# Performance work log

Measured on AMD Instinct MI355X. Metric: run time of the kernel, lower is better.

Reference implementation:

```python
import jax, jax.numpy as jnp
import numpy as np

B, N, K = 16, 4096, 32

def setup_inputs() -> dict:
    key = jax.random.key(0)
    k0, k1, k2, k3, k4, k5 = jax.random.split(key, 6)
    frames_rot = jax.random.normal(k0, (B, N, 3, 3), jnp.float32)
    frames_trans = jax.random.normal(k1, (B, N, 3), jnp.float32)
    pair_rot = jax.random.normal(k2, (B, N, K, 3, 3), jnp.float32)
    pair_trans = jax.random.normal(k3, (B, N, K, 3), jnp.float32)
    confidences = jax.random.uniform(k4, (B, N, K, 1), jnp.float32)
    topology = jax.random.randint(k5, (B, N, K), 0, N, jnp.int32)
    return {"frames_rot": frames_rot, "frames_trans": frames_trans,
            "pair_rot": pair_rot, "pair_trans": pair_trans,
            "confidences": confidences, "topology": topology}


def _proj_with_svd(m):
    """Kabsch projection of batched [..., 3, 3] matrices onto SO(3) (det=+1)."""
    u, s, vh = jnp.linalg.svd(m, full_matrices=False)
    V = jnp.swapaxes(vh, -1, -2)
    d = jnp.sign(jnp.linalg.det(jnp.matmul(V, jnp.swapaxes(u, -1, -2))))  # [...]
    d3 = jnp.concatenate([jnp.ones(d.shape + (2,), m.dtype), d[..., None]], axis=-1)  # diag(1,1,d)
    # rot = V @ diag(1,1,d) @ u^T
    return jnp.einsum('...ik,...k,...jk->...ij', V, d3, u)


def reference(frames_rot, frames_trans, pair_rot, pair_trans, confidences, topology):
    # gather neighbor frames T_j: [B,N,K,3,3] / [B,N,K,3]
    gather = jax.vmap(lambda f, t: f[t])
    Tj_rot = gather(frames_rot, topology)
    Tj_trans = gather(frames_trans, topology)

    # normalized confidences p_ij over neighbors K
    w = jnp.squeeze(confidences, axis=-1)             # [B,N,K]
    p = w / jnp.sum(w, axis=2, keepdims=True)         # [B,N,K]

    # compose rigids: T_j * T_ji
    comp_rot = jnp.einsum('bnkij,bnkjl->bnkil', Tj_rot, pair_rot)                 # [B,N,K,3,3]
    comp_trans = jnp.einsum('bnkij,bnkj->bnki', Tj_rot, pair_trans) + Tj_trans    # [B,N,K,3]

    # confidence-weighted average over neighbors
    avg_rot = jnp.einsum('bnk,bnkij->bnij', p, comp_rot)    # [B,N,3,3]
    avg_trans = jnp.einsum('bnk,bnki->bni', p, comp_trans)  # [B,N,3]

    # project averaged rot onto SO(3), then invert (transpose) as in the module
    rot = _proj_with_svd(avg_rot)
    rot_inv = jnp.swapaxes(rot, -1, -2)                     # invert_rots of a rotation

    # pack (rot 9 + trans 3) -> [B,N,12]
    return jnp.concatenate([rot_inv.reshape(B, N, 9), avg_trans], axis=-1)
```

## Files before the change

### kernel.cpp

```cpp
#include <hip/hip_runtime.h>
#include <math.h>

#define N_RES 4096
#define KNB 32
#define BN_TOTAL 65536

typedef float v4f __attribute__((ext_vector_type(4)));
typedef int v4i __attribute__((ext_vector_type(4)));

template <int p, int q>
__device__ __forceinline__ void jacobi_rot(float S[3][3], float V[3][3]) {
    float apq = S[p][q];
    if (fabsf(apq) > 1e-20f) {
        float app = S[p][p], aqq = S[q][q];
        float tau = (aqq - app) / (2.0f * apq);
        float tt = (tau >= 0.0f ? 1.0f : -1.0f) / (fabsf(tau) + sqrtf(1.0f + tau * tau));
        float c = 1.0f / sqrtf(1.0f + tt * tt);
        float s = tt * c;
#pragma unroll
        for (int i = 0; i < 3; i++) {
            float Sip = S[i][p], Siq = S[i][q];
            S[i][p] = c * Sip - s * Siq;
            S[i][q] = s * Sip + c * Siq;
        }
#pragma unroll
        for (int i = 0; i < 3; i++) {
            float Spi = S[p][i], Sqi = S[q][i];
            S[p][i] = c * Spi - s * Sqi;
            S[q][i] = s * Spi + c * Sqi;
        }
#pragma unroll
        for (int i = 0; i < 3; i++) {
            float Vip = V[i][p], Viq = V[i][q];
            V[i][p] = c * Vip - s * Viq;
            V[i][q] = s * Vip + c * Viq;
        }
    }
}

template <int A, int Bc>
__device__ __forceinline__ void sort_pair(float lam[3], float V[3][3]) {
    if (lam[A] < lam[Bc]) {
        float tl = lam[A]; lam[A] = lam[Bc]; lam[Bc] = tl;
#pragma unroll
        for (int i = 0; i < 3; i++) {
            float tv = V[i][A]; V[i][A] = V[i][Bc]; V[i][Bc] = tv;
        }
    }
}

__device__ __forceinline__ void project_and_store(const float M[3][3],
                                                  float t0, float t1, float t2,
                                                  float* outp) {
    float S[3][3];
#pragma unroll
    for (int i = 0; i < 3; i++)
#pragma unroll
        for (int j = 0; j < 3; j++)
            S[i][j] = M[0][i] * M[0][j] + M[1][i] * M[1][j] + M[2][i] * M[2][j];
    float V[3][3] = {{1, 0, 0}, {0, 1, 0}, {0, 0, 1}};

#pragma unroll
    for (int sweep = 0; sweep < 4; sweep++) {
        jacobi_rot<0, 1>(S, V);
        jacobi_rot<0, 2>(S, V);
        jacobi_rot<1, 2>(S, V);
    }

    float lam[3] = {S[0][0], S[1][1], S[2][2]};
    sort_pair<0, 1>(lam, V);
    sort_pair<1, 2>(lam, V);
    sort_pair<0, 1>(lam, V);

    float detV = V[0][0] * (V[1][1] * V[2][2] - V[1][2] * V[2][1]) -
                 V[0][1] * (V[1][0] * V[2][2] - V[1][2] * V[2][0]) +
                 V[0][2] * (V[1][0] * V[2][1] - V[1][1] * V[2][0]);
    if (detV < 0.0f) { V[0][2] = -V[0][2]; V[1][2] = -V[1][2]; V[2][2] = -V[2][2]; }

    float Bm[3][3];
#pragma unroll
    for (int i = 0; i < 3; i++)
#pragma unroll
        for (int j = 0; j < 3; j++)
            Bm[i][j] = M[i][0] * V[0][j] + M[i][1] * V[1][j] + M[i][2] * V[2][j];

    float u0[3] = {Bm[0][0], Bm[1][0], Bm[2][0]};
    float n0 = u0[0] * u0[0] + u0[1] * u0[1] + u0[2] * u0[2];
    float rn0 = 1.0f / sqrtf(fmaxf(n0, 1e-24f));
    u0[0] *= rn0; u0[1] *= rn0; u0[2] *= rn0;

    float b1[3] = {Bm[0][1], Bm[1][1], Bm[2][1]};
    float d01 = u0[0] * b1[0] + u0[1] * b1[1] + u0[2] * b1[2];
    float u1[3] = {b1[0] - d01 * u0[0], b1[1] - d01 * u0[1], b1[2] - d01 * u0[2]};
    float n1 = u1[0] * u1[0] + u1[1] * u1[1] + u1[2] * u1[2];
    float rn1 = 1.0f / sqrtf(fmaxf(n1, 1e-24f));
    u1[0] *= rn1; u1[1] *= rn1; u1[2] *= rn1;

    float u2[3] = {u0[1] * u1[2] - u0[2] * u1[1],
                   u0[2] * u1[0] - u0[0] * u1[2],
                   u0[0] * u1[1] - u0[1] * u1[0]};

    float R[9];
#pragma unroll
    for (int i = 0; i < 3; i++) {
        float Ui0 = (i == 0 ? u0[0] : (i == 1 ? u0[1] : u0[2]));
        float Ui1 = (i == 0 ? u1[0] : (i == 1 ? u1[1] : u1[2]));
        float Ui2 = (i == 0 ? u2[0] : (i == 1 ? u2[1] : u2[2]));
#pragma unroll
        for (int j = 0; j < 3; j++)
            R[i * 3 + j] = Ui0 * V[j][0] + Ui1 * V[j][1] + Ui2 * V[j][2];
    }

    v4f* o4 = (v4f*)outp;
    o4[0] = (v4f){R[0], R[1], R[2], R[3]};
    o4[1] = (v4f){R[4], R[5], R[6], R[7]};
    o4[2] = (v4f){R[8], t0, t1, t2};
}

__global__ __launch_bounds__(256) void repack_kernel(
    const float* __restrict__ frames_rot,
    const float* __restrict__ frames_trans,
    float* __restrict__ pk)
{
    int row = blockIdx.x * 256 + threadIdx.x;
    const float* fr = frames_rot + (size_t)row * 9;
    const float* ft = frames_trans + (size_t)row * 3;
    v4f* o = (v4f*)(pk + (size_t)row * 16);
    o[0] = (v4f){fr[0], fr[1], fr[2], fr[3]};
    o[1] = (v4f){fr[4], fr[5], fr[6], fr[7]};
    o[2] = (v4f){fr[8], ft[0], ft[1], ft[2]};
}

__global__ __launch_bounds__(256) void accum_kernel(
    const float* __restrict__ pk,
    const float* __restrict__ pair_rot,
    const float* __restrict__ pair_trans,
    const float* __restrict__ conf,
    const int* __restrict__ topo,
    float* __restrict__ acc)
{
    __shared__ float lds[4 * 768];

    int tid = threadIdx.x;
    int wid = tid >> 6;
    int L = tid & 63;
    int bid = blockIdx.x;

    int xcd = bid & 7;
    int slot = bid >> 3;
    int batch = xcd + ((slot >> 9) << 3);
    int within = slot & 511;
    int elem0 = batch * N_RES + within * 8 + wid * 2;

    int h = L >> 5;
    int k = L & 31;
    int elem_g = elem0 + h;

    float* wlds = lds + wid * 768;

    size_t nidx = (size_t)elem0 * KNB + L;
    float w = __builtin_nontemporal_load(conf + nidx);
    int j = __builtin_nontemporal_load(topo + nidx);

    const v4f* rg = (const v4f*)(pair_rot + (size_t)elem0 * (KNB * 9));
    for (int s = L; s < 144; s += 64) {
        v4f v = __builtin_nontemporal_load(rg + s);
        *(v4f*)(wlds + 4 * s) = v;
    }
    const v4f* tg = (const v4f*)(pair_trans + (size_t)elem0 * (KNB * 3));
    if (L < 48) {
        v4f v = __builtin_nontemporal_load(tg + L);
        *(v4f*)(wlds + 576 + 4 * L) = v;
    }

    const v4f* row = (const v4f*)(pk + ((size_t)batch * N_RES + (size_t)j) * 16);
    v4f fa = row[0], fb = row[1], fc = row[2];
    float r[9] = {fa.x, fa.y, fa.z, fa.w, fb.x, fb.y, fb.z, fb.w, fc.x};
    float tj0 = fc.y, tj1 = fc.z, tj2 = fc.w;

    const float* pr = wlds + h * 288 + k * 9;
    float p[9];
#pragma unroll
    for (int c = 0; c < 9; c++) p[c] = pr[c];
    const float* pt = wlds + 576 + h * 96 + k * 3;
    float q0 = pt[0], q1 = pt[1], q2 = pt[2];

    float Macc[9], tacc[3];
#pragma unroll
    for (int i = 0; i < 3; i++) {
#pragma unroll
        for (int l = 0; l < 3; l++) {
            Macc[i * 3 + l] = w * (r[i * 3 + 0] * p[0 * 3 + l] +
                                   r[i * 3 + 1] * p[1 * 3 + l] +
                                   r[i * 3 + 2] * p[2 * 3 + l]);
        }
        float tji = (i == 0 ? tj0 : (i == 1 ? tj1 : tj2));
        tacc[i] = w * (r[i * 3 + 0] * q0 + r[i * 3 + 1] * q1 +
                       r[i * 3 + 2] * q2 + tji);
    }
    float wsum = w;

#pragma unroll
    for (int st = 1; st <= 16; st <<= 1) {
#pragma unroll
        for (int i = 0; i < 9; i++) Macc[i] += __shfl_xor(Macc[i], st);
#pragma unroll
        for (int i = 0; i < 3; i++) tacc[i] += __shfl_xor(tacc[i], st);
        wsum += __shfl_xor(wsum, st);
    }

    if (k == 0) {
        v4f* o = (v4f*)(acc + (size_t)elem_g * 16);
        o[0] = (v4f){Macc[0], Macc[1], Macc[2], Macc[3]};
        o[1] = (v4f){Macc[4], Macc[5], Macc[6], Macc[7]};
        o[2] = (v4f){Macc[8], tacc[0], tacc[1], tacc[2]};
        o[3] = (v4f){wsum, 0.0f, 0.0f, 0.0f};
    }
}

__global__ __launch_bounds__(256) void solve_kernel(
    const float* __restrict__ acc,
    float* __restrict__ out)
{
    int elem = blockIdx.x * 256 + threadIdx.x;
    const v4f* a4 = (const v4f*)(acc + (size_t)elem * 16);
    v4f A0 = a4[0], A1 = a4[1], A2 = a4[2], A3 = a4[3];
    float inv_w = 1.0f / fmaxf(A3.x, 1e-20f);
    float M[3][3] = {{A0.x * inv_w, A0.y * inv_w, A0.z * inv_w},
                     {A0.w * inv_w, A1.x * inv_w, A1.y * inv_w},
                     {A1.z * inv_w, A1.w * inv_w, A2.x * inv_w}};
    float t0 = A2.y * inv_w, t1 = A2.z * inv_w, t2 = A2.w * inv_w;
    project_and_store(M, t0, t1, t2, out + (size_t)elem * 12);
}

__global__ __launch_bounds__(256) void fused_kernel(
    const float* __restrict__ frames_rot, const float* __restrict__ frames_trans,
    const float* __restrict__ pair_rot, const float* __restrict__ pair_trans,
    const float* __restrict__ conf, const int* __restrict__ topo,
    float* __restrict__ out)
{
    int tid = threadIdx.x;
    int bid = blockIdx.x;
    int xcd = bid & 7;
    int slot = bid >> 3;
    int batch = xcd + ((slot >> 7) << 3);
    int chunk = slot & 127;
    int elem = batch * N_RES + chunk * 32 + (tid >> 3);
    int t = tid & 7;

    const float* fr_b = frames_rot + (size_t)batch * N_RES * 9;
    const float* ft_b = frames_trans + (size_t)batch * N_RES * 3;

    size_t kbase = (size_t)elem * KNB + (size_t)t * 4;
    const v4f* pr4 = (const v4f*)(pair_rot + kbase * 9);
    const v4f* pt4 = (const v4f*)(pair_trans + kbase * 3);
    const v4f* cf4 = (const v4f*)(conf + kbase);
    const v4i* tp4 = (const v4i*)(topo + kbase);

    float prl[36];
#pragma unroll
    for (int i = 0; i < 9; i++) {
        v4f v = __builtin_nontemporal_load(pr4 + i);
        prl[4 * i] = v.x; prl[4 * i + 1] = v.y; prl[4 * i + 2] = v.z; prl[4 * i + 3] = v.w;
    }
    float ptl[12];
#pragma unroll
    for (int i = 0; i < 3; i++) {
        v4f v = __builtin_nontemporal_load(pt4 + i);
        ptl[4 * i] = v.x; ptl[4 * i + 1] = v.y; ptl[4 * i + 2] = v.z; ptl[4 * i + 3] = v.w;
    }
    v4f wv = __builtin_nontemporal_load(cf4);
    float wl[4] = {wv.x, wv.y, wv.z, wv.w};
    v4i jv = __builtin_nontemporal_load(tp4);
    int jl[4] = {jv.x, jv.y, jv.z, jv.w};

    float Macc[9] = {0, 0, 0, 0, 0, 0, 0, 0, 0};
    float tacc[3] = {0, 0, 0};
    float wsum = 0.0f;

#pragma unroll
    for (int kk = 0; kk < 4; kk++) {
        int j = jl[kk];
        const float* Rj = fr_b + j * 9;
        const float* Tj = ft_b + j * 3;
        float r[9];
#pragma unroll
        for (int i = 0; i < 9; i++) r[i] = Rj[i];
        float tj[3];
#pragma unroll
        for (int i = 0; i < 3; i++) tj[i] = Tj[i];
        float w = wl[kk];
        const float* pr = prl + kk * 9;
        const float* pt = ptl + kk * 3;
#pragma unroll
        for (int i = 0; i < 3; i++) {
#pragma unroll
            for (int l = 0; l < 3; l++) {
                float cij = r[i * 3] * pr[l] + r[i * 3 + 1] * pr[3 + l] + r[i * 3 + 2] * pr[6 + l];
                Macc[i * 3 + l] += w * cij;
            }
            float ct = r[i * 3] * pt[0] + r[i * 3 + 1] * pt[1] + r[i * 3 + 2] * pt[2] + tj[i];
            tacc[i] += w * ct;
        }
        wsum += w;
    }

#pragma unroll
    for (int st = 1; st <= 4; st <<= 1) {
#pragma unroll
        for (int i = 0; i < 9; i++) Macc[i] += __shfl_xor(Macc[i], st);
#pragma unroll
        for (int i = 0; i < 3; i++) tacc[i] += __shfl_xor(tacc[i], st);
        wsum += __shfl_xor(wsum, st);
    }

    float inv_w = 1.0f / fmaxf(wsum, 1e-20f);
    float M[3][3];
#pragma unroll
    for (int i = 0; i < 3; i++)
#pragma unroll
        for (int j = 0; j < 3; j++) M[i][j] = Macc[i * 3 + j] * inv_w;

    if (t == 0)
        project_and_store(M, tacc[0] * inv_w, tacc[1] * inv_w, tacc[2] * inv_w,
                          out + (size_t)elem * 12);
}

extern "C" void kernel_launch(void* const* d_in, const int* in_sizes, int n_in,
                              void* d_out, int out_size, void* d_ws, size_t ws_size,
                              hipStream_t stream) {
    const float* frames_rot = (const float*)d_in[0];
    const float* frames_trans = (const float*)d_in[1];
    const float* pair_rot = (const float*)d_in[2];
    const float* pair_trans = (const float*)d_in[3];
    const float* conf = (const float*)d_in[4];
    const int* topo = (const int*)d_in[5];
    float* out = (float*)d_out;

    const size_t PK_BYTES = (size_t)BN_TOTAL * 16 * sizeof(float);
    const size_t ACC_BYTES = (size_t)BN_TOTAL * 16 * sizeof(float);
    const size_t need = PK_BYTES + ACC_BYTES;

    if (ws_size >= need) {
        float* pk = (float*)d_ws;
        float* acc = (float*)((char*)d_ws + PK_BYTES);
        hipLaunchKernelGGL(repack_kernel, dim3(BN_TOTAL / 256), dim3(256), 0, stream,
                           frames_rot, frames_trans, pk);
        hipLaunchKernelGGL(accum_kernel, dim3(BN_TOTAL / 8), dim3(256), 0, stream,
                           pk, pair_rot, pair_trans, conf, topo, acc);
        hipLaunchKernelGGL(solve_kernel, dim3(BN_TOTAL / 256), dim3(256), 0, stream,
                           acc, out);
    } else {
        hipLaunchKernelGGL(fused_kernel, dim3(BN_TOTAL * 8 / 256), dim3(256), 0, stream,
                           frames_rot, frames_trans, pair_rot, pair_trans, conf, topo, out);
    }
}
```

Baseline: 169.1 us.

## Write per-group partial sums from accum kernel and reduce them in solve

```diff
diff --git a/kernel.cpp b/kernel.cpp
--- a/kernel.cpp
+++ b/kernel.cpp
@@ -137,9 +137,9 @@
     const float* __restrict__ pair_trans,
     const float* __restrict__ conf,
     const int* __restrict__ topo,
-    float* __restrict__ acc)
+    float* __restrict__ part)
 {
-    __shared__ float lds[4 * 768];
+    __shared__ float lds[4 * 576];
 
     int tid = threadIdx.x;
     int wid = tid >> 6;
@@ -156,21 +156,25 @@
     int k = L & 31;
     int elem_g = elem0 + h;
 
-    float* wlds = lds + wid * 768;
+    float* wlds = lds + wid * 576;
 
     size_t nidx = (size_t)elem0 * KNB + L;
     float w = __builtin_nontemporal_load(conf + nidx);
     int j = __builtin_nontemporal_load(topo + nidx);
 
+    const float* tgp = pair_trans + nidx * 3;
+    float q0 = __builtin_nontemporal_load(tgp + 0);
+    float q1 = __builtin_nontemporal_load(tgp + 1);
+    float q2 = __builtin_nontemporal_load(tgp + 2);
+
     const v4f* rg = (const v4f*)(pair_rot + (size_t)elem0 * (KNB * 9));
-    for (int s = L; s < 144; s += 64) {
-        v4f v = __builtin_nontemporal_load(rg + s);
-        *(v4f*)(wlds + 4 * s) = v;
-    }
-    const v4f* tg = (const v4f*)(pair_trans + (size_t)elem0 * (KNB * 3));
-    if (L < 48) {
-        v4f v = __builtin_nontemporal_load(tg + L);
-        *(v4f*)(wlds + 576 + 4 * L) = v;
+#pragma unroll
+    for (int s = 0; s < 3; s++) {
+        int i = L + 64 * s;
+        if (i < 144) {
+            v4f v = __builtin_nontemporal_load(rg + i);
+            *(v4f*)(wlds + 4 * i) = v;
+        }
     }
 
     const v4f* row = (const v4f*)(pk + ((size_t)batch * N_RES + (size_t)j) * 16);
@@ -178,12 +182,10 @@
     float r[9] = {fa.x, fa.y, fa.z, fa.w, fb.x, fb.y, fb.z, fb.w, fc.x};
     float tj0 = fc.y, tj1 = fc.z, tj2 = fc.w;
 
-    const float* pr = wlds + h * 288 + k * 9;
+    const float* pr = wlds + 9 * L;
     float p[9];
 #pragma unroll
     for (int c = 0; c < 9; c++) p[c] = pr[c];
-    const float* pt = wlds + 576 + h * 96 + k * 3;
-    float q0 = pt[0], q1 = pt[1], q2 = pt[2];
 
     float Macc[9], tacc[3];
 #pragma unroll
@@ -201,7 +203,7 @@
     float wsum = w;
 
 #pragma unroll
-    for (int st = 1; st <= 16; st <<= 1) {
+    for (int st = 1; st <= 2; st <<= 1) {
 #pragma unroll
         for (int i = 0; i < 9; i++) Macc[i] += __shfl_xor(Macc[i], st);
 #pragma unroll
@@ -209,8 +211,9 @@
         wsum += __shfl_xor(wsum, st);
     }
 
-    if (k == 0) {
-        v4f* o = (v4f*)(acc + (size_t)elem_g * 16);
+    if ((k & 3) == 0) {
+        int grp = k >> 2;
+        v4f* o = (v4f*)(part + ((size_t)elem_g * 8 + grp) * 16);
         o[0] = (v4f){Macc[0], Macc[1], Macc[2], Macc[3]};
         o[1] = (v4f){Macc[4], Macc[5], Macc[6], Macc[7]};
         o[2] = (v4f){Macc[8], tacc[0], tacc[1], tacc[2]};
@@ -219,17 +222,25 @@
 }
 
 __global__ __launch_bounds__(256) void solve_kernel(
-    const float* __restrict__ acc,
+    const float* __restrict__ part,
     float* __restrict__ out)
 {
     int elem = blockIdx.x * 256 + threadIdx.x;
-    const v4f* a4 = (const v4f*)(acc + (size_t)elem * 16);
-    v4f A0 = a4[0], A1 = a4[1], A2 = a4[2], A3 = a4[3];
-    float inv_w = 1.0f / fmaxf(A3.x, 1e-20f);
-    float M[3][3] = {{A0.x * inv_w, A0.y * inv_w, A0.z * inv_w},
-                     {A0.w * inv_w, A1.x * inv_w, A1.y * inv_w},
-                     {A1.z * inv_w, A1.w * inv_w, A2.x * inv_w}};
-    float t0 = A2.y * inv_w, t1 = A2.z * inv_w, t2 = A2.w * inv_w;
+    const v4f* p4 = (const v4f*)(part + (size_t)elem * 128);
+    v4f s0 = {0, 0, 0, 0}, s1 = {0, 0, 0, 0}, s2 = {0, 0, 0, 0};
+    float sw = 0.0f;
+#pragma unroll
+    for (int t = 0; t < 8; t++) {
+        s0 += p4[t * 4 + 0];
+        s1 += p4[t * 4 + 1];
+        s2 += p4[t * 4 + 2];
+        sw += p4[t * 4 + 3].x;
+    }
+    float inv_w = 1.0f / fmaxf(sw, 1e-20f);
+    float M[3][3] = {{s0.x * inv_w, s0.y * inv_w, s0.z * inv_w},
+                     {s0.w * inv_w, s1.x * inv_w, s1.y * inv_w},
+                     {s1.z * inv_w, s1.w * inv_w, s2.x * inv_w}};
+    float t0 = s2.y * inv_w, t1 = s2.z * inv_w, t2 = s2.w * inv_w;
     project_and_store(M, t0, t1, t2, out + (size_t)elem * 12);
 }
 
@@ -338,18 +349,18 @@
     float* out = (float*)d_out;
 
     const size_t PK_BYTES = (size_t)BN_TOTAL * 16 * sizeof(float);
-    const size_t ACC_BYTES = (size_t)BN_TOTAL * 16 * sizeof(float);
-    const size_t need = PK_BYTES + ACC_BYTES;
+    const size_t PART_BYTES = (size_t)BN_TOTAL * 8 * 16 * sizeof(float);
+    const size_t need = PK_BYTES + PART_BYTES;
 
     if (ws_size >= need) {
         float* pk = (float*)d_ws;
-        float* acc = (float*)((char*)d_ws + PK_BYTES);
+        float* part = (float*)((char*)d_ws + PK_BYTES);
         hipLaunchKernelGGL(repack_kernel, dim3(BN_TOTAL / 256), dim3(256), 0, stream,
                            frames_rot, frames_trans, pk);
         hipLaunchKernelGGL(accum_kernel, dim3(BN_TOTAL / 8), dim3(256), 0, stream,
-                           pk, pair_rot, pair_trans, conf, topo, acc);
+                           pk, pair_rot, pair_trans, conf, topo, part);
         hipLaunchKernelGGL(solve_kernel, dim3(BN_TOTAL / 256), dim3(256), 0, stream,
-                           acc, out);
+                           part, out);
     } else {
         hipLaunchKernelGGL(fused_kernel, dim3(BN_TOTAL * 8 / 256), dim3(256), 0, stream,
                            frames_rot, frames_trans, pair_rot, pair_trans, conf, topo, out);
```

Result: slower. 177.1 us (+4.7%).
